# Kernel tuning notes

Hardware: AMD Instinct MI355X
Metric: run time of the kernel (lower is better)

The kernel has to match this reference:

```python
import jax, jax.numpy as jnp
import numpy as np

N = 4096          # nproteins
IN_F = 512        # in_features
OUT_F = 64        # out_features
ALPHA = 0.2       # leakyrelu slope
EPS = 1e-5        # batchnorm eps
NEG = -9e15       # mask fill value from the original code


def setup_inputs() -> dict:
    key = jax.random.key(0)
    k = jax.random.split(key, 5)
    h = jax.random.normal(k[0], (N, IN_F), dtype=jnp.float32)
    # sparse 0/1 adjacency (avg degree ~20) stored dense, as the module expects
    adj = (jax.random.uniform(k[1], (N, N)) < 0.005).astype(jnp.float32)
    half = IN_F // 2
    # xavier_uniform with gain=1.414 ~ U(-b, b), b = gain*sqrt(6/(fan_in+fan_out))
    b_w = 1.414 * np.sqrt(6.0 / (half + OUT_F))
    W1 = jax.random.uniform(k[2], (half, OUT_F), minval=-b_w, maxval=b_w, dtype=jnp.float32)
    W2 = jax.random.uniform(k[3], (half, OUT_F), minval=-b_w, maxval=b_w, dtype=jnp.float32)
    b_a = 1.414 * np.sqrt(6.0 / (2 * OUT_F + 1))
    a = jax.random.uniform(k[4], (2 * OUT_F, 1), minval=-b_a, maxval=b_a, dtype=jnp.float32)
    gamma = jnp.ones((2 * OUT_F,), dtype=jnp.float32)   # bn2 weight
    beta = jnp.zeros((2 * OUT_F,), dtype=jnp.float32)   # bn2 bias
    return {"h": h, "adj": adj, "W1": W1, "W2": W2, "a": a, "gamma": gamma, "beta": beta}


def _lrelu(x):
    return jnp.where(x > 0, x, ALPHA * x)


def reference(h, adj, W1, W2, a, gamma, beta):
    d = h.shape[1] // 2
    Wh1 = h[:, :d] @ W1          # [N, F]
    Wh2 = h[:, d:] @ W2          # [N, F]

    def prep(Wh):
        s1 = Wh @ a[:OUT_F]      # [N, 1]
        s2 = Wh @ a[OUT_F:]      # [N, 1]
        return _lrelu(s1 + s2.T)  # [N, N]

    e1 = prep(Wh1)
    e2 = prep(Wh2)

    adj2 = adj @ adj                               # 2-hop counts [N, N]
    adj2 = adj2 - jnp.diag(jnp.diag(adj2))         # zero the diagonal

    att1 = jax.nn.softmax(jnp.where(adj > 0, e1, NEG), axis=1)
    h_prime1 = att1 @ Wh1                          # [N, F]
    att2 = jax.nn.softmax(jnp.where(adj2 > 0, e2, NEG), axis=1)
    h_prime2 = att2 @ Wh2                          # [N, F]

    hp = jnp.concatenate([h_prime1, h_prime2], axis=-1)  # [N, 2F]
    # BatchNorm1d (training-mode batch stats, biased variance)
    mean = hp.mean(axis=0)
    var = hp.var(axis=0)
    out = gamma * (hp - mean) / jnp.sqrt(var + EPS) + beta
    return _lrelu(out)  # concat=True branch
```

## Files before the change

kernel.cpp:

```cpp
#include <hip/hip_runtime.h>
#include <hip/hip_bf16.h>

#define NN 4096
#define IN_F 512
#define HALF 256
#define FF 64
#define ALPHA 0.2f
#define EPSV 1e-5f
#define CAP1 256
#define CAP2 1024
#define WHB (NN / 8)

typedef unsigned long long u64;
typedef unsigned int u32;

__device__ __forceinline__ float lrelu(float x){ return x > 0.f ? x : ALPHA * x; }

__device__ __forceinline__ float wave_fmax(float v){
    #pragma unroll
    for (int off = 32; off; off >>= 1) v = fmaxf(v, __shfl_xor(v, off, 64));
    return v;
}
__device__ __forceinline__ float wave_fsum(float v){
    #pragma unroll
    for (int off = 32; off; off >>= 1) v += __shfl_xor(v, off, 64);
    return v;
}

__device__ __forceinline__ int build_idx(u64 bits, int lane, int cap, int* __restrict__ nbr){
    int pc = __popcll(bits);
    int scan = pc;
    #pragma unroll
    for (int off = 1; off < 64; off <<= 1) {
        int v = __shfl_up(scan, off, 64);
        if (lane >= off) scan += v;
    }
    int total = __shfl(scan, 63, 64);
    int pos = scan - pc;
    while (bits) {
        int b = __builtin_ctzll(bits);
        bits &= bits - 1;
        if (pos < cap) nbr[pos] = (lane << 6) | b;
        ++pos;
    }
    return total;
}

__global__ __launch_bounds__(256) void packwh_kernel(const float* __restrict__ adj,
                                                     u64* __restrict__ packA,
                                                     const float* __restrict__ h,
                                                     const float* __restrict__ W1,
                                                     const float* __restrict__ W2,
                                                     const float* __restrict__ a,
                                                     float* __restrict__ Wh1,
                                                     float* __restrict__ Wh2,
                                                     float* __restrict__ s11,
                                                     float* __restrict__ s12,
                                                     float* __restrict__ s21,
                                                     float* __restrict__ s22) {
    __shared__ float hs[8 * IN_F];
    int tid = threadIdx.x;
    if (blockIdx.x < NN) {
        int i = blockIdx.x;
        int wave = tid >> 6, lane = tid & 63;
        const float* row = adj + (size_t)i * NN;
        #pragma unroll
        for (int t = 0; t < NN / 256; ++t) {
            int col = t * 256 + tid;
            u64 m = __ballot(row[col] > 0.f);
            if (lane == 0) packA[(size_t)i * 64 + t * 4 + wave] = m;
        }
    } else {
        int r0 = (blockIdx.x - NN) * 8;
        const float4* hsrc = (const float4*)(h + (size_t)r0 * IN_F);
        float4* hdst = (float4*)hs;
        #pragma unroll
        for (int t = 0; t < 4; ++t) hdst[tid + 256 * t] = hsrc[tid + 256 * t];
        __syncthreads();

        int w = tid >> 6, f = tid & 63;
        int br2 = w >> 1;
        int rbase = (w & 1) * 4;
        const float* W = br2 ? W2 : W1;
        const float* hw = hs + rbase * IN_F + br2 * HALF;
        float acc0 = 0.f, acc1 = 0.f, acc2 = 0.f, acc3 = 0.f;
        #pragma unroll 4
        for (int k = 0; k < HALF; ++k) {
            float wt = W[k * FF + f];
            acc0 += hw[k] * wt;
            acc1 += hw[IN_F + k] * wt;
            acc2 += hw[2 * IN_F + k] * wt;
            acc3 += hw[3 * IN_F + k] * wt;
        }
        float* Wh = br2 ? Wh2 : Wh1;
        int rr = r0 + rbase;
        Wh[(size_t)(rr + 0) * FF + f] = acc0;
        Wh[(size_t)(rr + 1) * FF + f] = acc1;
        Wh[(size_t)(rr + 2) * FF + f] = acc2;
        Wh[(size_t)(rr + 3) * FF + f] = acc3;

        float a1 = a[f], a2 = a[64 + f];
        #pragma unroll
        for (int r = 0; r < 4; ++r) {
            float acc = (r == 0) ? acc0 : (r == 1) ? acc1 : (r == 2) ? acc2 : acc3;
            float v1 = acc * a1, v2 = acc * a2;
            #pragma unroll
            for (int off = 32; off; off >>= 1) {
                v1 += __shfl_down(v1, off, 64);
                v2 += __shfl_down(v2, off, 64);
            }
            if (f == 0) {
                if (br2 == 0) { s11[rr + r] = v1; s12[rr + r] = v2; }
                else          { s21[rr + r] = v1; s22[rr + r] = v2; }
            }
        }
    }
}

__global__ __launch_bounds__(256) void attn_kernel(const u64* __restrict__ packA,
                                                   const float* __restrict__ Wh1,
                                                   const float* __restrict__ Wh2,
                                                   const float* __restrict__ s11,
                                                   const float* __restrict__ s12,
                                                   const float* __restrict__ s21,
                                                   const float* __restrict__ s22,
                                                   float* __restrict__ hp) {
    __shared__ int   nbr1[CAP1];
    __shared__ float ev1[CAP1];
    __shared__ int   nbr2[CAP2];
    __shared__ float ev2[CAP2];
    __shared__ u64   maskw[3 * 64];
    __shared__ float red[8];
    __shared__ float partial[1024];
    __shared__ int   scnt1, scnt2;

    int i = blockIdx.x;
    int tid = threadIdx.x;
    int w = tid >> 6, lane = tid & 63;

    if (w == 0) {
        int t1 = build_idx(packA[(size_t)i * 64 + lane], lane, CAP1, nbr1);
        if (lane == 0) scnt1 = t1;
    }
    __syncthreads();
    int c1 = min(scnt1, CAP1);

    if (c1 > 0) {
        if (w == 0) {
            int c1p = (c1 + 15) & ~15;
            for (int n = c1 + lane; n < c1p; n += 64) { nbr1[n] = 0; ev1[n] = 0.f; }
            float s11i = s11[i];
            float lm = -3.4e38f;
            for (int n = lane; n < c1; n += 64) {
                float e = lrelu(s11i + s12[nbr1[n]]);
                ev1[n] = e;
                lm = fmaxf(lm, e);
            }
            float m = wave_fmax(lm);
            float ls = 0.f;
            for (int n = lane; n < c1; n += 64) {
                float p = __expf(ev1[n] - m);
                ev1[n] = p;
                ls += p;
            }
            float invZ = 1.f / wave_fsum(ls);
            int g = lane >> 4, fq = (lane & 15) << 2;
            float ax = 0.f, ay = 0.f, az = 0.f, aw = 0.f;
            for (int n = g * 4; n < c1p; n += 16) {
                int4   nb = *(const int4*)&nbr1[n];
                float4 wv = *(const float4*)&ev1[n];
                float4 q0 = *(const float4*)&Wh1[nb.x * FF + fq];
                float4 q1 = *(const float4*)&Wh1[nb.y * FF + fq];
                float4 q2 = *(const float4*)&Wh1[nb.z * FF + fq];
                float4 q3 = *(const float4*)&Wh1[nb.w * FF + fq];
                ax += wv.x * q0.x + wv.y * q1.x + wv.z * q2.x + wv.w * q3.x;
                ay += wv.x * q0.y + wv.y * q1.y + wv.z * q2.y + wv.w * q3.y;
                az += wv.x * q0.z + wv.y * q1.z + wv.z * q2.z + wv.w * q3.z;
                aw += wv.x * q0.w + wv.y * q1.w + wv.z * q2.w + wv.w * q3.w;
            }
            ax += __shfl_xor(ax, 16, 64); ax += __shfl_xor(ax, 32, 64);
            ay += __shfl_xor(ay, 16, 64); ay += __shfl_xor(ay, 32, 64);
            az += __shfl_xor(az, 16, 64); az += __shfl_xor(az, 32, 64);
            aw += __shfl_xor(aw, 16, 64); aw += __shfl_xor(aw, 32, 64);
            if (g == 0)
                *(float4*)&hp[(size_t)i * 128 + fq] =
                    make_float4(ax * invZ, ay * invZ, az * invZ, aw * invZ);
        } else {
            u64 m = 0;
            for (int n = w - 1; n < c1; n += 3)
                m |= packA[nbr1[n] * 64 + lane];
            maskw[(w - 1) * 64 + lane] = m;
        }
    } else {
        int g = tid >> 4, fq = (tid & 15) << 2;
        float ax = 0.f, ay = 0.f, az = 0.f, aw = 0.f;
        for (int n = g; n < NN; n += 16) {
            float4 v = *(const float4*)&Wh1[n * FF + fq];
            ax += v.x; ay += v.y; az += v.z; aw += v.w;
        }
        *(float4*)&partial[tid << 2] = make_float4(ax, ay, az, aw);
        if (w) maskw[(w - 1) * 64 + lane] = 0;
        __syncthreads();
        if (tid < 64) {
            float s = 0.f;
            #pragma unroll
            for (int g2 = 0; g2 < 16; ++g2) s += partial[g2 * 64 + tid];
            hp[(size_t)i * 128 + tid] = s * (1.f / NN);
        }
    }
    __syncthreads();

    if (w == 0) {
        u64 word = maskw[lane] | maskw[64 + lane] | maskw[128 + lane];
        if (lane == (i >> 6)) word &= ~(1ull << (i & 63));
        int t2 = build_idx(word, lane, CAP2, nbr2);
        if (lane == 0) scnt2 = t2;
    }
    __syncthreads();
    int c2 = min(scnt2, CAP2);
    int c2p = (c2 + 63) & ~63;

    float Z2inv;
    if (c2 > 0) {
        float s21i = s21[i];
        float lm = -3.4e38f;
        for (int n = tid; n < c2; n += 256) {
            float e = lrelu(s21i + s22[nbr2[n]]);
            ev2[n] = e;
            lm = fmaxf(lm, e);
        }
        lm = wave_fmax(lm);
        if (lane == 0) red[w] = lm;
        __syncthreads();
        float mx = fmaxf(fmaxf(red[0], red[1]), fmaxf(red[2], red[3]));
        float ls = 0.f;
        for (int n = tid; n < c2; n += 256) {
            float p = __expf(ev2[n] - mx);
            ev2[n] = p;
            ls += p;
        }
        for (int n = c2 + tid; n < c2p; n += 256) { ev2[n] = 0.f; nbr2[n] = 0; }
        ls = wave_fsum(ls);
        if (lane == 0) red[4 + w] = ls;
        __syncthreads();
        Z2inv = 1.f / (red[4] + red[5] + red[6] + red[7]);
    } else {
        Z2inv = 1.f / (float)NN;
    }

    int g = tid >> 4, fq = (tid & 15) << 2;
    float ax = 0.f, ay = 0.f, az = 0.f, aw = 0.f;
    if (c2 > 0) {
        for (int n = g * 4; n < c2p; n += 64) {
            int4   nb = *(const int4*)&nbr2[n];
            float4 wv = *(const float4*)&ev2[n];
            float4 q0 = *(const float4*)&Wh2[nb.x * FF + fq];
            float4 q1 = *(const float4*)&Wh2[nb.y * FF + fq];
            float4 q2 = *(const float4*)&Wh2[nb.z * FF + fq];
            float4 q3 = *(const float4*)&Wh2[nb.w * FF + fq];
            ax += wv.x * q0.x + wv.y * q1.x + wv.z * q2.x + wv.w * q3.x;
            ay += wv.x * q0.y + wv.y * q1.y + wv.z * q2.y + wv.w * q3.y;
            az += wv.x * q0.z + wv.y * q1.z + wv.z * q2.z + wv.w * q3.z;
            aw += wv.x * q0.w + wv.y * q1.w + wv.z * q2.w + wv.w * q3.w;
        }
    } else {
        for (int n = g; n < NN; n += 16) {
            float4 v = *(const float4*)&Wh2[n * FF + fq];
            ax += v.x; ay += v.y; az += v.z; aw += v.w;
        }
    }
    *(float4*)&partial[tid << 2] = make_float4(ax, ay, az, aw);
    __syncthreads();
    if (tid < 64) {
        float s = 0.f;
        #pragma unroll
        for (int g2 = 0; g2 < 16; ++g2) s += partial[g2 * 64 + tid];
        hp[(size_t)i * 128 + 64 + tid] = s * Z2inv;
    }
}

__global__ __launch_bounds__(256) void stats_kernel(const float* __restrict__ hp,
                                                    float* __restrict__ ps,
                                                    float* __restrict__ pq) {
    __shared__ float ls[128], lq[128];
    int tid = threadIdx.x;
    if (tid < 128) { ls[tid] = 0.f; lq[tid] = 0.f; }
    __syncthreads();
    float s0 = 0, s1 = 0, s2 = 0, s3 = 0, q0 = 0, q1 = 0, q2 = 0, q3 = 0;
    const float4* hp4 = (const float4*)hp;
    for (size_t idx = (size_t)blockIdx.x * 256 + tid; idx < (size_t)NN * 32;
         idx += (size_t)gridDim.x * 256) {
        float4 v = hp4[idx];
        s0 += v.x; q0 += v.x * v.x;
        s1 += v.y; q1 += v.y * v.y;
        s2 += v.z; q2 += v.z * v.z;
        s3 += v.w; q3 += v.w * v.w;
    }
    int cb = (tid & 31) << 2;
    atomicAdd(&ls[cb + 0], s0); atomicAdd(&lq[cb + 0], q0);
    atomicAdd(&ls[cb + 1], s1); atomicAdd(&lq[cb + 1], q1);
    atomicAdd(&ls[cb + 2], s2); atomicAdd(&lq[cb + 2], q2);
    atomicAdd(&ls[cb + 3], s3); atomicAdd(&lq[cb + 3], q3);
    __syncthreads();
    if (tid < 128) {
        ps[(size_t)blockIdx.x * 128 + tid] = ls[tid];
        pq[(size_t)blockIdx.x * 128 + tid] = lq[tid];
    }
}

__global__ __launch_bounds__(256) void finalize_kernel(const float* __restrict__ ps,
                                                       const float* __restrict__ pq,
                                                       float* __restrict__ colsum,
                                                       float* __restrict__ colsq) {
    int tid = threadIdx.x;
    const float* src = (tid < 128) ? ps : pq;
    int c = tid & 127;
    float s = 0.f;
    #pragma unroll 8
    for (int b = 0; b < 256; ++b) s += src[(size_t)b * 128 + c];
    if (tid < 128) colsum[c] = s;
    else           colsq[c]  = s;
}

__global__ __launch_bounds__(256) void norm_kernel(float* __restrict__ hp,
                                                   const float* __restrict__ colsum,
                                                   const float* __restrict__ colsq,
                                                   const float* __restrict__ gamma,
                                                   const float* __restrict__ beta) {
    size_t idx = (size_t)blockIdx.x * 256 + threadIdx.x;
    if (idx >= (size_t)NN * 32) return;
    int cb = (int)((idx << 2) & 127);
    float4 v = ((const float4*)hp)[idx];
    float r[4] = {v.x, v.y, v.z, v.w};
    #pragma unroll
    for (int t = 0; t < 4; ++t) {
        int c = cb + t;
        float mean = colsum[c] * (1.f / NN);
        float var = colsq[c] * (1.f / NN) - mean * mean;
        float inv = rsqrtf(var + EPSV);
        r[t] = lrelu((r[t] - mean) * inv * gamma[c] + beta[c]);
    }
    ((float4*)hp)[idx] = make_float4(r[0], r[1], r[2], r[3]);
}

extern "C" void kernel_launch(void* const* d_in, const int* in_sizes, int n_in,
                              void* d_out, int out_size, void* d_ws, size_t ws_size,
                              hipStream_t stream) {
    const float* h     = (const float*)d_in[0];
    const float* adj   = (const float*)d_in[1];
    const float* W1    = (const float*)d_in[2];
    const float* W2    = (const float*)d_in[3];
    const float* a     = (const float*)d_in[4];
    const float* gamma = (const float*)d_in[5];
    const float* beta  = (const float*)d_in[6];
    float* hp = (float*)d_out;

    u64* packA  = (u64*)d_ws;
    float* Wh1  = (float*)(packA + (size_t)NN * 64);
    float* Wh2  = Wh1 + (size_t)NN * FF;
    float* s11  = Wh2 + (size_t)NN * FF;
    float* s12  = s11 + NN;
    float* s21  = s12 + NN;
    float* s22  = s21 + NN;
    float* ps   = s22 + NN;
    float* pq   = ps + 256 * 128;
    float* colsum = pq + 256 * 128;
    float* colsq  = colsum + 128;

    packwh_kernel<<<NN + WHB, 256, 0, stream>>>(adj, packA, h, W1, W2, a,
                                                Wh1, Wh2, s11, s12, s21, s22);
    attn_kernel<<<NN, 256, 0, stream>>>(packA, Wh1, Wh2, s11, s12, s21, s22, hp);
    stats_kernel<<<256, 256, 0, stream>>>(hp, ps, pq);
    finalize_kernel<<<1, 256, 0, stream>>>(ps, pq, colsum, colsq);
    norm_kernel<<<(NN * 32 + 255) / 256, 256, 0, stream>>>(hp, colsum, colsq, gamma, beta);
}
```

Measured before the change: 183.3 us.

## Process one node per wave in attention, vectorize adj packing, fuse BN finalize

The attention kernel now gives each wave its own node, four nodes per block, with 16-bit neighbor indices in shared memory. This removes the block-wide syncs and the cross-wave mask/partial reductions. Adjacency packing reads float4 and builds 64-bit words through shuffles instead of scalar ballots. The BN finalize is folded into the normalize kernel, and the stats grid is halved, which drops one launch. Each wave now walks all two-hop neighbors serially with scalar-per-lane gathers, and CAP1 is halved, which risks truncating high-degree rows.

```diff
diff --git a/kernel.cpp b/kernel.cpp
--- a/kernel.cpp
+++ b/kernel.cpp
@@ -7,12 +7,13 @@
 #define FF 64
 #define ALPHA 0.2f
 #define EPSV 1e-5f
-#define CAP1 256
+#define CAP1 128
 #define CAP2 1024
 #define WHB (NN / 8)
 
 typedef unsigned long long u64;
 typedef unsigned int u32;
+typedef unsigned short u16;
 
 __device__ __forceinline__ float lrelu(float x){ return x > 0.f ? x : ALPHA * x; }
 
@@ -27,7 +28,7 @@
     return v;
 }
 
-__device__ __forceinline__ int build_idx(u64 bits, int lane, int cap, int* __restrict__ nbr){
+__device__ __forceinline__ int build_idx16(u64 bits, int lane, int cap, u16* __restrict__ nbr){
     int pc = __popcll(bits);
     int scan = pc;
     #pragma unroll
@@ -40,7 +41,7 @@
     while (bits) {
         int b = __builtin_ctzll(bits);
         bits &= bits - 1;
-        if (pos < cap) nbr[pos] = (lane << 6) | b;
+        if (pos < cap) nbr[pos] = (u16)((lane << 6) | b);
         ++pos;
     }
     return total;
@@ -62,13 +63,22 @@
     int tid = threadIdx.x;
     if (blockIdx.x < NN) {
         int i = blockIdx.x;
-        int wave = tid >> 6, lane = tid & 63;
-        const float* row = adj + (size_t)i * NN;
+        int lane = tid & 63;
+        int sh = (lane & 15) << 2;
+        const float4* row = (const float4*)(adj + (size_t)i * NN);
         #pragma unroll
-        for (int t = 0; t < NN / 256; ++t) {
-            int col = t * 256 + tid;
-            u64 m = __ballot(row[col] > 0.f);
-            if (lane == 0) packA[(size_t)i * 64 + t * 4 + wave] = m;
+        for (int t = 0; t < 4; ++t) {
+            int idx = t * 256 + tid;
+            float4 v = row[idx];
+            u32 nib = (u32)(v.x > 0.f) | ((u32)(v.y > 0.f) << 1) |
+                      ((u32)(v.z > 0.f) << 2) | ((u32)(v.w > 0.f) << 3);
+            u64 word = (u64)nib << sh;
+            word |= __shfl_xor(word, 1, 64);
+            word |= __shfl_xor(word, 2, 64);
+            word |= __shfl_xor(word, 4, 64);
+            word |= __shfl_xor(word, 8, 64);
+            if ((lane & 15) == 0)
+                packA[(size_t)i * 64 + (idx >> 4)] = word;
         }
     } else {
         int r0 = (blockIdx.x - NN) * 8;
@@ -125,158 +135,108 @@
                                                    const float* __restrict__ s21,
                                                    const float* __restrict__ s22,
                                                    float* __restrict__ hp) {
-    __shared__ int   nbr1[CAP1];
-    __shared__ float ev1[CAP1];
-    __shared__ int   nbr2[CAP2];
-    __shared__ float ev2[CAP2];
-    __shared__ u64   maskw[3 * 64];
-    __shared__ float red[8];
-    __shared__ float partial[1024];
-    __shared__ int   scnt1, scnt2;
-
-    int i = blockIdx.x;
+    __shared__ u16   nbr1s[4][CAP1];
+    __shared__ u16   nbr2s[4][CAP2];
+    __shared__ float evs[4][CAP2];
+
     int tid = threadIdx.x;
     int w = tid >> 6, lane = tid & 63;
-
-    if (w == 0) {
-        int t1 = build_idx(packA[(size_t)i * 64 + lane], lane, CAP1, nbr1);
-        if (lane == 0) scnt1 = t1;
-    }
-    __syncthreads();
-    int c1 = min(scnt1, CAP1);
-
+    int i = blockIdx.x * 4 + w;
+
+    u16*   nbr1 = nbr1s[w];
+    u16*   nbr2 = nbr2s[w];
+    float* ev   = evs[w];
+
+    int t1 = build_idx16(packA[(size_t)i * 64 + lane], lane, CAP1, nbr1);
+    int c1 = min(t1, CAP1);
+
+    float out1;
     if (c1 > 0) {
-        if (w == 0) {
-            int c1p = (c1 + 15) & ~15;
-            for (int n = c1 + lane; n < c1p; n += 64) { nbr1[n] = 0; ev1[n] = 0.f; }
-            float s11i = s11[i];
-            float lm = -3.4e38f;
-            for (int n = lane; n < c1; n += 64) {
-                float e = lrelu(s11i + s12[nbr1[n]]);
-                ev1[n] = e;
-                lm = fmaxf(lm, e);
-            }
-            float m = wave_fmax(lm);
-            float ls = 0.f;
-            for (int n = lane; n < c1; n += 64) {
-                float p = __expf(ev1[n] - m);
-                ev1[n] = p;
-                ls += p;
-            }
-            float invZ = 1.f / wave_fsum(ls);
-            int g = lane >> 4, fq = (lane & 15) << 2;
-            float ax = 0.f, ay = 0.f, az = 0.f, aw = 0.f;
-            for (int n = g * 4; n < c1p; n += 16) {
-                int4   nb = *(const int4*)&nbr1[n];
-                float4 wv = *(const float4*)&ev1[n];
-                float4 q0 = *(const float4*)&Wh1[nb.x * FF + fq];
-                float4 q1 = *(const float4*)&Wh1[nb.y * FF + fq];
-                float4 q2 = *(const float4*)&Wh1[nb.z * FF + fq];
-                float4 q3 = *(const float4*)&Wh1[nb.w * FF + fq];
-                ax += wv.x * q0.x + wv.y * q1.x + wv.z * q2.x + wv.w * q3.x;
-                ay += wv.x * q0.y + wv.y * q1.y + wv.z * q2.y + wv.w * q3.y;
-                az += wv.x * q0.z + wv.y * q1.z + wv.z * q2.z + wv.w * q3.z;
-                aw += wv.x * q0.w + wv.y * q1.w + wv.z * q2.w + wv.w * q3.w;
-            }
-            ax += __shfl_xor(ax, 16, 64); ax += __shfl_xor(ax, 32, 64);
-            ay += __shfl_xor(ay, 16, 64); ay += __shfl_xor(ay, 32, 64);
-            az += __shfl_xor(az, 16, 64); az += __shfl_xor(az, 32, 64);
-            aw += __shfl_xor(aw, 16, 64); aw += __shfl_xor(aw, 32, 64);
-            if (g == 0)
-                *(float4*)&hp[(size_t)i * 128 + fq] =
-                    make_float4(ax * invZ, ay * invZ, az * invZ, aw * invZ);
-        } else {
-            u64 m = 0;
-            for (int n = w - 1; n < c1; n += 3)
-                m |= packA[nbr1[n] * 64 + lane];
-            maskw[(w - 1) * 64 + lane] = m;
-        }
+        int c1p = (c1 + 3) & ~3;
+        if (lane < c1p - c1) { nbr1[c1 + lane] = 0; }
+        float s11i = s11[i];
+        float lm = -3.4e38f;
+        for (int n = lane; n < c1; n += 64) {
+            float e = lrelu(s11i + s12[nbr1[n]]);
+            ev[n] = e;
+            lm = fmaxf(lm, e);
+        }
+        float m = wave_fmax(lm);
+        float ls = 0.f;
+        for (int n = lane; n < c1; n += 64) {
+            float p = __expf(ev[n] - m);
+            ev[n] = p;
+            ls += p;
+        }
+        float invZ = 1.f / wave_fsum(ls);
+        if (lane < c1p - c1) { ev[c1 + lane] = 0.f; }
+        float a0 = 0.f, a1 = 0.f, a2 = 0.f, a3 = 0.f;
+        for (int n = 0; n < c1p; n += 4) {
+            ushort4 nb = *(const ushort4*)&nbr1[n];
+            float4  wv = *(const float4*)&ev[n];
+            a0 += wv.x * Wh1[(int)nb.x * FF + lane];
+            a1 += wv.y * Wh1[(int)nb.y * FF + lane];
+            a2 += wv.z * Wh1[(int)nb.z * FF + lane];
+            a3 += wv.w * Wh1[(int)nb.w * FF + lane];
+        }
+        out1 = (a0 + a1 + a2 + a3) * invZ;
     } else {
-        int g = tid >> 4, fq = (tid & 15) << 2;
-        float ax = 0.f, ay = 0.f, az = 0.f, aw = 0.f;
-        for (int n = g; n < NN; n += 16) {
-            float4 v = *(const float4*)&Wh1[n * FF + fq];
-            ax += v.x; ay += v.y; az += v.z; aw += v.w;
-        }
-        *(float4*)&partial[tid << 2] = make_float4(ax, ay, az, aw);
-        if (w) maskw[(w - 1) * 64 + lane] = 0;
-        __syncthreads();
-        if (tid < 64) {
-            float s = 0.f;
-            #pragma unroll
-            for (int g2 = 0; g2 < 16; ++g2) s += partial[g2 * 64 + tid];
-            hp[(size_t)i * 128 + tid] = s * (1.f / NN);
-        }
-    }
-    __syncthreads();
-
-    if (w == 0) {
-        u64 word = maskw[lane] | maskw[64 + lane] | maskw[128 + lane];
-        if (lane == (i >> 6)) word &= ~(1ull << (i & 63));
-        int t2 = build_idx(word, lane, CAP2, nbr2);
-        if (lane == 0) scnt2 = t2;
-    }
-    __syncthreads();
-    int c2 = min(scnt2, CAP2);
-    int c2p = (c2 + 63) & ~63;
-
-    float Z2inv;
+        float a0 = 0.f, a1 = 0.f;
+        for (int n = 0; n < NN; n += 2) {
+            a0 += Wh1[n * FF + lane];
+            a1 += Wh1[(n + 1) * FF + lane];
+        }
+        out1 = (a0 + a1) * (1.f / NN);
+    }
+    hp[(size_t)i * 128 + lane] = out1;
+
+    u64 word = 0;
+    for (int n = 0; n < c1; ++n)
+        word |= packA[(size_t)nbr1[n] * 64 + lane];
+    if (lane == (i >> 6)) word &= ~(1ull << (i & 63));
+
+    int t2 = build_idx16(word, lane, CAP2, nbr2);
+    int c2 = min(t2, CAP2);
+
+    float out2;
     if (c2 > 0) {
+        int c2p = (c2 + 3) & ~3;
+        if (lane < c2p - c2) { nbr2[c2 + lane] = 0; }
         float s21i = s21[i];
         float lm = -3.4e38f;
-        for (int n = tid; n < c2; n += 256) {
+        for (int n = lane; n < c2; n += 64) {
             float e = lrelu(s21i + s22[nbr2[n]]);
-            ev2[n] = e;
+            ev[n] = e;
             lm = fmaxf(lm, e);
         }
-        lm = wave_fmax(lm);
-        if (lane == 0) red[w] = lm;
-        __syncthreads();
-        float mx = fmaxf(fmaxf(red[0], red[1]), fmaxf(red[2], red[3]));
+        float m = wave_fmax(lm);
         float ls = 0.f;
-        for (int n = tid; n < c2; n += 256) {
-            float p = __expf(ev2[n] - mx);
-            ev2[n] = p;
+        for (int n = lane; n < c2; n += 64) {
+            float p = __expf(ev[n] - m);
+            ev[n] = p;
             ls += p;
         }
-        for (int n = c2 + tid; n < c2p; n += 256) { ev2[n] = 0.f; nbr2[n] = 0; }
-        ls = wave_fsum(ls);
-        if (lane == 0) red[4 + w] = ls;
-        __syncthreads();
-        Z2inv = 1.f / (red[4] + red[5] + red[6] + red[7]);
+        float invZ = 1.f / wave_fsum(ls);
+        if (lane < c2p - c2) { ev[c2 + lane] = 0.f; }
+        float a0 = 0.f, a1 = 0.f, a2 = 0.f, a3 = 0.f;
+        for (int n = 0; n < c2p; n += 4) {
+            ushort4 nb = *(const ushort4*)&nbr2[n];
+            float4  wv = *(const float4*)&ev[n];
+            a0 += wv.x * Wh2[(int)nb.x * FF + lane];
+            a1 += wv.y * Wh2[(int)nb.y * FF + lane];
+            a2 += wv.z * Wh2[(int)nb.z * FF + lane];
+            a3 += wv.w * Wh2[(int)nb.w * FF + lane];
+        }
+        out2 = (a0 + a1 + a2 + a3) * invZ;
     } else {
-        Z2inv = 1.f / (float)NN;
-    }
-
-    int g = tid >> 4, fq = (tid & 15) << 2;
-    float ax = 0.f, ay = 0.f, az = 0.f, aw = 0.f;
-    if (c2 > 0) {
-        for (int n = g * 4; n < c2p; n += 64) {
-            int4   nb = *(const int4*)&nbr2[n];
-            float4 wv = *(const float4*)&ev2[n];
-            float4 q0 = *(const float4*)&Wh2[nb.x * FF + fq];
-            float4 q1 = *(const float4*)&Wh2[nb.y * FF + fq];
-            float4 q2 = *(const float4*)&Wh2[nb.z * FF + fq];
-            float4 q3 = *(const float4*)&Wh2[nb.w * FF + fq];
-            ax += wv.x * q0.x + wv.y * q1.x + wv.z * q2.x + wv.w * q3.x;
-            ay += wv.x * q0.y + wv.y * q1.y + wv.z * q2.y + wv.w * q3.y;
-            az += wv.x * q0.z + wv.y * q1.z + wv.z * q2.z + wv.w * q3.z;
-            aw += wv.x * q0.w + wv.y * q1.w + wv.z * q2.w + wv.w * q3.w;
-        }
-    } else {
-        for (int n = g; n < NN; n += 16) {
-            float4 v = *(const float4*)&Wh2[n * FF + fq];
-            ax += v.x; ay += v.y; az += v.z; aw += v.w;
-        }
-    }
-    *(float4*)&partial[tid << 2] = make_float4(ax, ay, az, aw);
-    __syncthreads();
-    if (tid < 64) {
-        float s = 0.f;
-        #pragma unroll
-        for (int g2 = 0; g2 < 16; ++g2) s += partial[g2 * 64 + tid];
-        hp[(size_t)i * 128 + 64 + tid] = s * Z2inv;
-    }
+        float a0 = 0.f, a1 = 0.f;
+        for (int n = 0; n < NN; n += 2) {
+            a0 += Wh2[n * FF + lane];
+            a1 += Wh2[(n + 1) * FF + lane];
+        }
+        out2 = (a0 + a1) * (1.f / NN);
+    }
+    hp[(size_t)i * 128 + 64 + lane] = out2;
 }
 
 __global__ __launch_bounds__(256) void stats_kernel(const float* __restrict__ hp,
@@ -308,39 +268,43 @@
     }
 }
 
-__global__ __launch_bounds__(256) void finalize_kernel(const float* __restrict__ ps,
-                                                       const float* __restrict__ pq,
-                                                       float* __restrict__ colsum,
-                                                       float* __restrict__ colsq) {
+__global__ __launch_bounds__(256) void normf_kernel(float* __restrict__ hp,
+                                                    const float* __restrict__ ps,
+                                                    const float* __restrict__ pq,
+                                                    const float* __restrict__ gamma,
+                                                    const float* __restrict__ beta) {
+    __shared__ float csum[256];
+    __shared__ float cmean[128], cginv[128];
     int tid = threadIdx.x;
-    const float* src = (tid < 128) ? ps : pq;
-    int c = tid & 127;
-    float s = 0.f;
-    #pragma unroll 8
-    for (int b = 0; b < 256; ++b) s += src[(size_t)b * 128 + c];
-    if (tid < 128) colsum[c] = s;
-    else           colsq[c]  = s;
-}
-
-__global__ __launch_bounds__(256) void norm_kernel(float* __restrict__ hp,
-                                                   const float* __restrict__ colsum,
-                                                   const float* __restrict__ colsq,
-                                                   const float* __restrict__ gamma,
-                                                   const float* __restrict__ beta) {
-    size_t idx = (size_t)blockIdx.x * 256 + threadIdx.x;
-    if (idx >= (size_t)NN * 32) return;
-    int cb = (int)((idx << 2) & 127);
-    float4 v = ((const float4*)hp)[idx];
-    float r[4] = {v.x, v.y, v.z, v.w};
-    #pragma unroll
-    for (int t = 0; t < 4; ++t) {
-        int c = cb + t;
-        float mean = colsum[c] * (1.f / NN);
-        float var = colsq[c] * (1.f / NN) - mean * mean;
-        float inv = rsqrtf(var + EPSV);
-        r[t] = lrelu((r[t] - mean) * inv * gamma[c] + beta[c]);
-    }
-    ((float4*)hp)[idx] = make_float4(r[0], r[1], r[2], r[3]);
+    {
+        const float* src = (tid < 128) ? ps : pq;
+        int c = tid & 127;
+        float s = 0.f;
+        #pragma unroll 8
+        for (int b = 0; b < 128; ++b) s += src[b * 128 + c];
+        csum[tid] = s;
+    }
+    __syncthreads();
+    if (tid < 128) {
+        float mean = csum[tid] * (1.f / NN);
+        float var = csum[128 + tid] * (1.f / NN) - mean * mean;
+        cmean[tid] = mean;
+        cginv[tid] = rsqrtf(var + EPSV) * gamma[tid];
+    }
+    __syncthreads();
+
+    size_t idx = (size_t)blockIdx.x * 256 + tid;
+    if (idx < (size_t)NN * 32) {
+        int cb = (int)((idx << 2) & 127);
+        float4 v = ((const float4*)hp)[idx];
+        float r[4] = {v.x, v.y, v.z, v.w};
+        #pragma unroll
+        for (int t = 0; t < 4; ++t) {
+            int c = cb + t;
+            r[t] = lrelu((r[t] - cmean[c]) * cginv[c] + beta[c]);
+        }
+        ((float4*)hp)[idx] = make_float4(r[0], r[1], r[2], r[3]);
+    }
 }
 
 extern "C" void kernel_launch(void* const* d_in, const int* in_sizes, int n_in,
@@ -363,14 +327,11 @@
     float* s21  = s12 + NN;
     float* s22  = s21 + NN;
     float* ps   = s22 + NN;
-    float* pq   = ps + 256 * 128;
-    float* colsum = pq + 256 * 128;
-    float* colsq  = colsum + 128;
+    float* pq   = ps + 128 * 128;
 
     packwh_kernel<<<NN + WHB, 256, 0, stream>>>(adj, packA, h, W1, W2, a,
                                                 Wh1, Wh2, s11, s12, s21, s22);
-    attn_kernel<<<NN, 256, 0, stream>>>(packA, Wh1, Wh2, s11, s12, s21, s22, hp);
-    stats_kernel<<<256, 256, 0, stream>>>(hp, ps, pq);
-    finalize_kernel<<<1, 256, 0, stream>>>(ps, pq, colsum, colsq);
-    norm_kernel<<<(NN * 32 + 255) / 256, 256, 0, stream>>>(hp, colsum, colsq, gamma, beta);
-}
+    attn_kernel<<<NN / 4, 256, 0, stream>>>(packA, Wh1, Wh2, s11, s12, s21, s22, hp);
+    stats_kernel<<<128, 256, 0, stream>>>(hp, ps, pq);
+    normf_kernel<<<(NN * 32 + 255) / 256, 256, 0, stream>>>(hp, ps, pq, gamma, beta);
+}
```

New measurement: 168.9 us. -7.8%, faster.
